# Kernel tuning notes

Measured on AMD Instinct MI355X. Metric: run time of the kernel, lower is better.

The kernel has to match this reference:

```python
import jax, jax.numpy as jnp
import numpy as np

NEG_SLOPE = 0.2  # PyG GATConv default negative_slope


def _gat_layer(x, src, dst, W, a_src, a_dst, b, num_nodes):
    # x: [N, Fin] -> h: [N, Fout]
    h = x @ W
    # per-node attention logits (heads=1)
    alpha_s = h @ a_src  # [N]
    alpha_d = h @ a_dst  # [N]
    # edge scores e_ij = LeakyReLU(a_src . h_j + a_dst . h_i), j=src, i=dst
    e = alpha_s[src] + alpha_d[dst]
    e = jnp.where(e >= 0, e, NEG_SLOPE * e)
    # segment softmax over edges sharing the same destination node
    e_max = jax.ops.segment_max(e, dst, num_segments=num_nodes)  # [N]
    w = jnp.exp(e - e_max[dst])  # [E]
    denom = jax.ops.segment_sum(w, dst, num_segments=num_nodes)  # [N]
    alpha = w / denom[dst]  # [E]
    # weighted scatter-sum of source messages into destinations
    out = jax.ops.segment_sum(h[src] * alpha[:, None], dst, num_segments=num_nodes)
    return out + b


def _add_self_loops(edge_index, num_nodes):
    loops = jnp.arange(num_nodes, dtype=edge_index.dtype)
    src = jnp.concatenate([edge_index[0], loops])
    dst = jnp.concatenate([edge_index[1], loops])
    return src, dst


def setup_inputs() -> dict:
    key = jax.random.key(0)
    ks = jax.random.split(key, 8)
    N, E, F_in, F_hid, F_out = 50000, 800000, 128, 128, 64
    inp = {
        "node_features": jax.random.normal(ks[0], (N, F_in), dtype=jnp.float32),
        "edge_index": jax.random.randint(ks[1], (2, E), 0, N, dtype=jnp.int32),
        "W1": jax.random.normal(ks[2], (F_in, F_hid), dtype=jnp.float32) / np.sqrt(F_in),
        "a_src1": jax.random.normal(ks[3], (F_hid,), dtype=jnp.float32) / np.sqrt(F_hid),
        "a_dst1": jax.random.normal(ks[4], (F_hid,), dtype=jnp.float32) / np.sqrt(F_hid),
        "b1": jnp.zeros((F_hid,), dtype=jnp.float32),
        "W2": jax.random.normal(ks[5], (F_hid, F_out), dtype=jnp.float32) / np.sqrt(F_hid),
        "a_src2": jax.random.normal(ks[6], (F_out,), dtype=jnp.float32) / np.sqrt(F_out),
        "a_dst2": jax.random.normal(ks[7], (F_out,), dtype=jnp.float32) / np.sqrt(F_out),
        "b2": jnp.zeros((F_out,), dtype=jnp.float32),
    }
    return inp


def reference(node_features, edge_index, W1, a_src1, a_dst1, b1, W2, a_src2, a_dst2, b2):
    num_nodes = node_features.shape[0]
    src, dst = _add_self_loops(edge_index, num_nodes)
    x = _gat_layer(node_features, src, dst, W1, a_src1, a_dst1, b1, num_nodes)
    x = jax.nn.relu(x)
    x = _gat_layer(x, src, dst, W2, a_src2, a_dst2, b2, num_nodes)
    return x
```

## Files before the change

### kernel.cpp

```cpp
#include <hip/hip_runtime.h>
#include <hip/hip_fp16.h>
#include <cstddef>

#define NEG_SLOPE 0.2f
#define TILE 4096
#define CSR_CAP 6144

typedef _Float16 h8 __attribute__((ext_vector_type(8)));
typedef _Float16 h4 __attribute__((ext_vector_type(4)));
typedef float f4 __attribute__((ext_vector_type(4)));

__device__ __forceinline__ float leaky(float x) { return x >= 0.f ? x : NEG_SLOPE * x; }

__device__ __forceinline__ int wave_iscan(int v, int lane) {
#pragma unroll
    for (int off = 1; off < 64; off <<= 1) {
        int t = __shfl_up(v, off);
        if (lane >= off) v += t;
    }
    return v;
}

__global__ __launch_bounds__(256) void prep(
    const float* __restrict__ W1, const float* __restrict__ W2,
    _Float16* __restrict__ W1t, _Float16* __restrict__ W2t,
    int* __restrict__ bfill)
{
    const int b = blockIdx.x;
    const int tid = threadIdx.x;
    if (b == 0) bfill[tid] = 0;
    if (b < 8) {
        for (int i = b * 2048 + tid; i < (b + 1) * 2048; i += 256) {
            int n = i >> 7, k = i & 127;
            W1t[n * 128 + k] = (_Float16)W1[k * 128 + n];
        }
    } else {
        const int bb = b - 8;
        for (int i = bb * 2048 + tid; i < (bb + 1) * 2048; i += 256) {
            int n = i >> 7, k = i & 127;
            W2t[n * 128 + k] = (_Float16)W2[k * 64 + n];
        }
    }
}

__global__ __launch_bounds__(256) void gemm1_scatter(
    const float* __restrict__ x, const _Float16* __restrict__ Wg,
    const float* __restrict__ a_s, const float* __restrict__ a_d,
    _Float16* __restrict__ hh, float* __restrict__ alphaS, float* __restrict__ alphaD,
    int N, int nblk_gemm,
    const int* __restrict__ src, const int* __restrict__ dst,
    int* __restrict__ bfill, unsigned* __restrict__ staging, int cap, int E)
{
    constexpr int K = 128;
    constexpr int LDK = K + 8;
    constexpr int F = 128;
    constexpr int NT = F / 16;

    __shared__ union {
        struct { _Float16 As[64 * LDK]; _Float16 Wt[F * LDK]; } g;
        struct {
            int lcnt[256]; int loff[256]; int gbase[256]; int ws[4];
            unsigned pairs[TILE]; unsigned char bkt[TILE];
        } s;
    } u;

    const int tid = threadIdx.x;

    if (blockIdx.x < (unsigned)nblk_gemm) {
        const int wave = tid >> 6;
        const int lane = tid & 63;
        const int q = lane >> 4;
        const int c = lane & 15;
        const int rowb = blockIdx.x * 64;

        for (int i = tid; i < 64 * (K / 4); i += 256) {
            int r = i >> 5, c4 = i & 31;
            int gr = rowb + r;
            float4 v = (gr < N) ? *(const float4*)(x + (size_t)gr * K + c4 * 4)
                                : make_float4(0.f, 0.f, 0.f, 0.f);
            h4 hv = { (_Float16)v.x, (_Float16)v.y, (_Float16)v.z, (_Float16)v.w };
            *(h4*)(u.g.As + r * LDK + c4 * 4) = hv;
        }
        for (int i = tid; i < F * (K / 8); i += 256) {
            int n = i >> 4, k8 = i & 15;
            *(h8*)(u.g.Wt + n * LDK + k8 * 8) = *(const h8*)(Wg + n * 128 + k8 * 8);
        }
        __syncthreads();

        f4 acc[NT];
#pragma unroll
        for (int nt = 0; nt < NT; nt++) acc[nt] = (f4)0.f;

        const _Float16* aw = u.g.As + (wave * 16 + c) * LDK + q * 8;
#pragma unroll
        for (int kt = 0; kt < 4; kt++) {
            h8 af = *(const h8*)(aw + kt * 32);
#pragma unroll
            for (int nt = 0; nt < NT; nt++) {
                h8 bf = *(const h8*)(u.g.Wt + (nt * 16 + c) * LDK + kt * 32 + q * 8);
                acc[nt] = __builtin_amdgcn_mfma_f32_16x16x32_f16(af, bf, acc[nt], 0, 0, 0);
            }
        }

        float asl[NT], adl[NT];
#pragma unroll
        for (int nt = 0; nt < NT; nt++) {
            asl[nt] = a_s[nt * 16 + c];
            adl[nt] = a_d[nt * 16 + c];
        }
        const int row0 = rowb + wave * 16 + q * 4;
#pragma unroll
        for (int r = 0; r < 4; r++) {
            int row = row0 + r;
            if (row < N) {
                float ps = 0.f, pd = 0.f;
#pragma unroll
                for (int nt = 0; nt < NT; nt++) {
                    float v = acc[nt][r];
                    hh[(size_t)row * F + nt * 16 + c] = (_Float16)v;
                    ps += v * asl[nt];
                    pd += v * adl[nt];
                }
#pragma unroll
                for (int off = 8; off >= 1; off >>= 1) {
                    ps += __shfl_down(ps, off, 16);
                    pd += __shfl_down(pd, off, 16);
                }
                if (c == 0) { alphaS[row] = ps; alphaD[row] = pd; }
            }
        }
    } else {
        const int base = (blockIdx.x - nblk_gemm) * TILE;
        const int vt = min(TILE, E - base);

        u.s.lcnt[tid] = 0;
        __syncthreads();

        int d[TILE / 256], s[TILE / 256], r[TILE / 256];
#pragma unroll
        for (int j = 0; j < TILE / 256; j++) {
            int idx = base + j * 256 + tid;
            if (idx < E) {
                d[j] = dst[idx]; s[j] = src[idx];
                r[j] = atomicAdd(&u.s.lcnt[d[j] >> 8], 1);
            } else d[j] = -1;
        }
        __syncthreads();
        {
            int lane = tid & 63, wid = tid >> 6;
            int v = u.s.lcnt[tid];
            int incl = wave_iscan(v, lane);
            if (lane == 63) u.s.ws[wid] = incl;
            __syncthreads();
            int woff = 0;
            for (int w = 0; w < wid; w++) woff += u.s.ws[w];
            u.s.loff[tid] = woff + incl - v;
        }
        __syncthreads();
        {
            int c = u.s.lcnt[tid];
            if (c > 0) u.s.gbase[tid] = tid * cap + atomicAdd(&bfill[tid], c);
        }
        __syncthreads();
#pragma unroll
        for (int j = 0; j < TILE / 256; j++) {
            if (d[j] >= 0) {
                int b = d[j] >> 8;
                int slot = u.s.loff[b] + r[j];
                u.s.pairs[slot] = ((unsigned)d[j] << 16) | (unsigned)s[j];
                u.s.bkt[slot] = (unsigned char)b;
            }
        }
        __syncthreads();
        for (int slot = tid; slot < vt; slot += 256) {
            int b = u.s.bkt[slot];
            staging[u.s.gbase[b] + (slot - u.s.loff[b])] = u.s.pairs[slot];
        }
    }
}

__global__ __launch_bounds__(512) void bucket_to_csr(
    const unsigned* __restrict__ staging, const int* __restrict__ bfill,
    int* __restrict__ row_start, int* __restrict__ row_end,
    int* __restrict__ src_sorted, int cap, int N)
{
    __shared__ unsigned lp[CSR_CAP];
    __shared__ int lcnt[256], loff[256], lfill[256];
    __shared__ int ws[4];
    const int tid = threadIdx.x;
    const int b = blockIdx.x;
    const int beg = b * cap;
    const int len = bfill[b];

    if (tid < 256) lcnt[tid] = 0;
    __syncthreads();
    for (int p = tid; p < len; p += 512) {
        unsigned u = staging[beg + p];
        lp[p] = u;
        atomicAdd(&lcnt[(u >> 16) & 255], 1);
    }
    __syncthreads();
    {
        int lane = tid & 63, wid = tid >> 6;
        int v = 0, incl = 0;
        if (tid < 256) {
            v = lcnt[tid];
            incl = wave_iscan(v, lane);
            if (lane == 63) ws[wid] = incl;
        }
        __syncthreads();
        if (tid < 256) {
            int woff = 0;
            for (int w = 0; w < wid; w++) woff += ws[w];
            int excl = woff + incl - v;
            loff[tid] = excl;
            lfill[tid] = excl;
            int node = (b << 8) + tid;
            if (node < N) { row_start[node] = beg + excl; row_end[node] = beg + excl + v; }
        }
    }
    __syncthreads();
    for (int p = tid; p < len; p += 512) {
        unsigned u = lp[p];
        int pos = atomicAdd(&lfill[(u >> 16) & 255], 1);
        src_sorted[beg + pos] = (int)(u & 0xFFFFu);
    }
}

template <int F, typename IT>
__global__ __launch_bounds__(256) void gemm_mfma(
    const IT* __restrict__ x, const _Float16* __restrict__ Wg,
    const float* __restrict__ a_s, const float* __restrict__ a_d,
    _Float16* __restrict__ hh, float* __restrict__ alphaS, float* __restrict__ alphaD,
    int N)
{
    constexpr int K = 128;
    constexpr int LDK = K + 8;
    constexpr int NT = F / 16;

    __shared__ _Float16 As[64 * LDK];
    __shared__ _Float16 Wt[F * LDK];

    const int tid = threadIdx.x;
    const int wave = tid >> 6;
    const int lane = tid & 63;
    const int q = lane >> 4;
    const int c = lane & 15;
    const int rowb = blockIdx.x * 64;

    if constexpr (sizeof(IT) == 4) {
        for (int i = tid; i < 64 * (K / 4); i += 256) {
            int r = i >> 5, c4 = i & 31;
            int gr = rowb + r;
            float4 v = (gr < N) ? *(const float4*)((const float*)x + (size_t)gr * K + c4 * 4)
                                : make_float4(0.f, 0.f, 0.f, 0.f);
            h4 hv = { (_Float16)v.x, (_Float16)v.y, (_Float16)v.z, (_Float16)v.w };
            *(h4*)(As + r * LDK + c4 * 4) = hv;
        }
    } else {
        for (int i = tid; i < 64 * (K / 8); i += 256) {
            int r = i >> 4, c8 = i & 15;
            int gr = rowb + r;
            h8 v;
            if (gr < N) v = *(const h8*)((const _Float16*)x + (size_t)gr * K + c8 * 8);
            else        v = (h8)(_Float16)0.f;
            *(h8*)(As + r * LDK + c8 * 8) = v;
        }
    }
    for (int i = tid; i < F * (K / 8); i += 256) {
        int n = i >> 4, k8 = i & 15;
        *(h8*)(Wt + n * LDK + k8 * 8) = *(const h8*)(Wg + n * 128 + k8 * 8);
    }
    __syncthreads();

    f4 acc[NT];
#pragma unroll
    for (int nt = 0; nt < NT; nt++) acc[nt] = (f4)0.f;

    const _Float16* aw = As + (wave * 16 + c) * LDK + q * 8;
#pragma unroll
    for (int kt = 0; kt < 4; kt++) {
        h8 af = *(const h8*)(aw + kt * 32);
#pragma unroll
        for (int nt = 0; nt < NT; nt++) {
            h8 bf = *(const h8*)(Wt + (nt * 16 + c) * LDK + kt * 32 + q * 8);
            acc[nt] = __builtin_amdgcn_mfma_f32_16x16x32_f16(af, bf, acc[nt], 0, 0, 0);
        }
    }

    float asl[NT], adl[NT];
#pragma unroll
    for (int nt = 0; nt < NT; nt++) {
        asl[nt] = a_s[nt * 16 + c];
        adl[nt] = a_d[nt * 16 + c];
    }
    const int row0 = rowb + wave * 16 + q * 4;
#pragma unroll
    for (int r = 0; r < 4; r++) {
        int row = row0 + r;
        if (row < N) {
            float ps = 0.f, pd = 0.f;
#pragma unroll
            for (int nt = 0; nt < NT; nt++) {
                float v = acc[nt][r];
                hh[(size_t)row * F + nt * 16 + c] = (_Float16)v;
                ps += v * asl[nt];
                pd += v * adl[nt];
            }
#pragma unroll
            for (int off = 8; off >= 1; off >>= 1) {
                ps += __shfl_down(ps, off, 16);
                pd += __shfl_down(pd, off, 16);
            }
            if (c == 0) { alphaS[row] = ps; alphaD[row] = pd; }
        }
    }
}

#define EDGE_BODY(SV, ACC, DEN)                                              \
    if (SV >= 0) {                                                           \
        float w = __expf(leaky(aS[SV] + adi));                               \
        uint4 uu = *(const uint4*)(hh + (size_t)SV * F + l * 8);             \
        const __half2* hp = (const __half2*)&uu;                             \
        _Pragma("unroll")                                                    \
        for (int q = 0; q < 4; q++) {                                        \
            float2 f = __half22float2(hp[q]);                                \
            ACC[q * 2] += w * f.x; ACC[q * 2 + 1] += w * f.y;                 \
        }                                                                    \
        DEN += w;                                                            \
    }

template <int F, int NS, bool RELU, typename OT>
__global__ __launch_bounds__(256) void gat_aggregate(
    const int* __restrict__ row_start, const int* __restrict__ row_end,
    const int* __restrict__ src_sorted, const __half* __restrict__ hh,
    const float* __restrict__ aS, const float* __restrict__ aD,
    const float* __restrict__ bias, OT* __restrict__ out, int N)
{
    constexpr int LPE = F / 8;
    constexpr int EPW = 64 / LPE;
    constexpr int WIN = NS * EPW;

    const int i = blockIdx.x * 4 + (threadIdx.x >> 6);
    if (i >= N) return;
    const int lane = threadIdx.x & 63;
    const int sub = lane / LPE;
    const int l = lane % LPE;

    const float adi = aD[i];
    const int start = row_start[i];
    const int end = row_end[i];

    float accA[8], accB[8];
#pragma unroll
    for (int q = 0; q < 8; q++) { accA[q] = 0.f; accB[q] = 0.f; }
    float denA = 0.f, denB = 0.f;

    int e = start + sub;
    int s0 = (e + 0 * EPW < end) ? src_sorted[e + 0 * EPW] : -1;
    int s1 = (e + 1 * EPW < end) ? src_sorted[e + 1 * EPW] : -1;
    int s2 = (e + 2 * EPW < end) ? src_sorted[e + 2 * EPW] : -1;
    int s3 = (e + 3 * EPW < end) ? src_sorted[e + 3 * EPW] : -1;
    int s4 = -1, s5 = -1, s6 = -1, s7 = -1;
    if constexpr (NS == 8) {
        s4 = (e + 4 * EPW < end) ? src_sorted[e + 4 * EPW] : -1;
        s5 = (e + 5 * EPW < end) ? src_sorted[e + 5 * EPW] : -1;
        s6 = (e + 6 * EPW < end) ? src_sorted[e + 6 * EPW] : -1;
        s7 = (e + 7 * EPW < end) ? src_sorted[e + 7 * EPW] : -1;
    }

    while (s0 >= 0) {
        int eb = e + WIN;
        int n0 = (eb + 0 * EPW < end) ? src_sorted[eb + 0 * EPW] : -1;
        int n1 = (eb + 1 * EPW < end) ? src_sorted[eb + 1 * EPW] : -1;
        int n2 = (eb + 2 * EPW < end) ? src_sorted[eb + 2 * EPW] : -1;
        int n3 = (eb + 3 * EPW < end) ? src_sorted[eb + 3 * EPW] : -1;
        int n4 = -1, n5 = -1, n6 = -1, n7 = -1;
        if constexpr (NS == 8) {
            n4 = (eb + 4 * EPW < end) ? src_sorted[eb + 4 * EPW] : -1;
            n5 = (eb + 5 * EPW < end) ? src_sorted[eb + 5 * EPW] : -1;
            n6 = (eb + 6 * EPW < end) ? src_sorted[eb + 6 * EPW] : -1;
            n7 = (eb + 7 * EPW < end) ? src_sorted[eb + 7 * EPW] : -1;
        }

        EDGE_BODY(s0, accA, denA)
        EDGE_BODY(s1, accB, denB)
        EDGE_BODY(s2, accA, denA)
        EDGE_BODY(s3, accB, denB)
        if constexpr (NS == 8) {
            EDGE_BODY(s4, accA, denA)
            EDGE_BODY(s5, accB, denB)
            EDGE_BODY(s6, accA, denA)
            EDGE_BODY(s7, accB, denB)
        }

        e = eb;
        s0 = n0; s1 = n1; s2 = n2; s3 = n3;
        if constexpr (NS == 8) { s4 = n4; s5 = n5; s6 = n6; s7 = n7; }
    }

    float acc[8];
#pragma unroll
    for (int q = 0; q < 8; q++) acc[q] = accA[q] + accB[q];
    float denom = denA + denB;

#pragma unroll
    for (int off = 32; off >= LPE; off >>= 1) {
#pragma unroll
        for (int q = 0; q < 8; q++) acc[q] += __shfl_down(acc[q], off);
        denom += __shfl_down(denom, off);
    }

    if (sub == 0) {
        float wsf = __expf(leaky(aS[i] + adi));
        uint4 u = *(const uint4*)(hh + (size_t)i * F + l * 8);
        const __half2* hp = (const __half2*)&u;
        float inv = 1.f / (denom + wsf);
        float4 b0 = *(const float4*)(bias + l * 8);
        float4 b1 = *(const float4*)(bias + l * 8 + 4);
        float o[8];
#pragma unroll
        for (int q = 0; q < 4; q++) {
            float2 f = __half22float2(hp[q]);
            o[q * 2]     = (acc[q * 2]     + wsf * f.x) * inv;
            o[q * 2 + 1] = (acc[q * 2 + 1] + wsf * f.y) * inv;
        }
        o[0] += b0.x; o[1] += b0.y; o[2] += b0.z; o[3] += b0.w;
        o[4] += b1.x; o[5] += b1.y; o[6] += b1.z; o[7] += b1.w;
        if (RELU) {
#pragma unroll
            for (int q = 0; q < 8; q++) o[q] = fmaxf(o[q], 0.f);
        }
        if constexpr (sizeof(OT) == 2) {
            __half2 qh[4];
            qh[0] = __floats2half2_rn(o[0], o[1]);
            qh[1] = __floats2half2_rn(o[2], o[3]);
            qh[2] = __floats2half2_rn(o[4], o[5]);
            qh[3] = __floats2half2_rn(o[6], o[7]);
            *(uint4*)((__half*)out + (size_t)i * F + l * 8) = *(uint4*)qh;
        } else {
            *(float4*)((float*)out + (size_t)i * F + l * 8)     = make_float4(o[0], o[1], o[2], o[3]);
            *(float4*)((float*)out + (size_t)i * F + l * 8 + 4) = make_float4(o[4], o[5], o[6], o[7]);
        }
    }
}

extern "C" void kernel_launch(void* const* d_in, const int* in_sizes, int n_in,
                              void* d_out, int out_size, void* d_ws, size_t ws_size,
                              hipStream_t stream)
{
    const float* x   = (const float*)d_in[0];
    const int*   ei  = (const int*)d_in[1];
    const float* W1  = (const float*)d_in[2];
    const float* aS1 = (const float*)d_in[3];
    const float* aD1 = (const float*)d_in[4];
    const float* b1  = (const float*)d_in[5];
    const float* W2  = (const float*)d_in[6];
    const float* aS2 = (const float*)d_in[7];
    const float* aD2 = (const float*)d_in[8];
    const float* b2  = (const float*)d_in[9];

    const int K = 128, F1 = 128, F2 = 64;
    const int N = in_sizes[0] / K;
    const int E = in_sizes[1] / 2;
    const int* src = ei;
    const int* dst = ei + E;

    const int Np = (N + 4) & ~3;
    const int NB = (N + 255) >> 8;
    const int nbt = (E + TILE - 1) / TILE;
    const int nblk_gemm = (N + 63) / 64;
    int cap = (((E / NB) * 3) / 2 + 255) & ~255;
    if (cap > CSR_CAP) cap = CSR_CAP;

    char* wsb = (char*)d_ws;
    int* bfill        = (int*)wsb;      wsb += 256 * 4;
    _Float16* W1t     = (_Float16*)wsb; wsb += 128 * 128 * 2;
    _Float16* W2t     = (_Float16*)wsb; wsb += 64 * 128 * 2;
    int* row_start    = (int*)wsb;      wsb += (size_t)Np * 4;
    int* row_end      = (int*)wsb;      wsb += (size_t)Np * 4;
    unsigned* staging = (unsigned*)wsb; wsb += (size_t)NB * CSR_CAP * 4;
    int* src_sorted   = (int*)wsb;      wsb += (size_t)NB * CSR_CAP * 4;
    _Float16* hh1     = (_Float16*)wsb; wsb += (size_t)N * F1 * 2;
    _Float16* x2h     = (_Float16*)wsb; wsb += (size_t)N * F1 * 2;
    _Float16* hh2     = (_Float16*)wsb; wsb += (size_t)N * F2 * 2;
    float* as_        = (float*)wsb;    wsb += (size_t)Np * 4;
    float* ad_        = (float*)wsb;    wsb += (size_t)Np * 4;
    float* as2_       = (float*)wsb;    wsb += (size_t)Np * 4;
    float* ad2_       = (float*)wsb;    wsb += (size_t)Np * 4;

    dim3 blk(256);

    prep<<<dim3(12), blk, 0, stream>>>(W1, W2, W1t, W2t, bfill);

    gemm1_scatter<<<dim3(nblk_gemm + nbt), blk, 0, stream>>>(
        x, W1t, aS1, aD1, hh1, as_, ad_, N, nblk_gemm,
        src, dst, bfill, staging, cap, E);

    bucket_to_csr<<<dim3(NB), dim3(512), 0, stream>>>(staging, bfill, row_start, row_end,
                                                      src_sorted, cap, N);

    gat_aggregate<F1, 8, true, __half><<<dim3((N + 3) / 4), blk, 0, stream>>>(
        row_start, row_end, src_sorted, (const __half*)hh1, as_, ad_, b1,
        (__half*)x2h, N);

    gemm_mfma<F2, _Float16><<<dim3((N + 63) / 64), blk, 0, stream>>>(
        x2h, W2t, aS2, aD2, hh2, as2_, ad2_, N);

    gat_aggregate<F2, 4, false, float><<<dim3((N + 3) / 4), blk, 0, stream>>>(
        row_start, row_end, src_sorted, (const __half*)hh2, as2_, ad2_, b2,
        (float*)d_out, N);
}
```

Before: 194.9 us.

## Precompute layer-1 edge weights and denominators during CSR build

The CSR construction kernel now computes each edge's unnormalized attention weight for layer 1, stores it next to the source index as an int2, and accumulates per-destination denominators in shared memory. The layer-1 aggregation then reads these precomputed weights instead of gathering alpha_s and calling exp per edge. The cost is a doubled edge-array footprint (8 bytes per edge), which layer 2 also pays because it reads only the .x field of the same int2 array. The max-subtraction was already absent, so numerics are unchanged apart from the order of the denominator sums.

```diff
diff --git a/kernel.cpp b/kernel.cpp
--- a/kernel.cpp
+++ b/kernel.cpp
@@ -182,17 +182,20 @@
 __global__ __launch_bounds__(512) void bucket_to_csr(
     const unsigned* __restrict__ staging, const int* __restrict__ bfill,
     int* __restrict__ row_start, int* __restrict__ row_end,
-    int* __restrict__ src_sorted, int cap, int N)
+    int2* __restrict__ sw_sorted, float* __restrict__ denom1,
+    const float* __restrict__ aS1, const float* __restrict__ aD1,
+    int cap, int N)
 {
     __shared__ unsigned lp[CSR_CAP];
     __shared__ int lcnt[256], loff[256], lfill[256];
+    __shared__ float dsum[256];
     __shared__ int ws[4];
     const int tid = threadIdx.x;
     const int b = blockIdx.x;
     const int beg = b * cap;
     const int len = bfill[b];
 
-    if (tid < 256) lcnt[tid] = 0;
+    if (tid < 256) { lcnt[tid] = 0; dsum[tid] = 0.f; }
     __syncthreads();
     for (int p = tid; p < len; p += 512) {
         unsigned u = staging[beg + p];
@@ -222,8 +225,17 @@
     __syncthreads();
     for (int p = tid; p < len; p += 512) {
         unsigned u = lp[p];
-        int pos = atomicAdd(&lfill[(u >> 16) & 255], 1);
-        src_sorted[beg + pos] = (int)(u & 0xFFFFu);
+        int node = (u >> 16) & 255;
+        int s = (int)(u & 0xFFFFu);
+        int pos = atomicAdd(&lfill[node], 1);
+        float w = __expf(leaky(aS1[s] + aD1[(b << 8) + node]));
+        sw_sorted[beg + pos] = make_int2(s, __float_as_int(w));
+        atomicAdd(&dsum[node], w);
+    }
+    __syncthreads();
+    if (tid < 256) {
+        int node = (b << 8) + tid;
+        if (node < N) denom1[node] = dsum[tid];
     }
 }
 
@@ -317,10 +329,99 @@
     }
 }
 
+__global__ __launch_bounds__(256) void gat_aggregate_pre(
+    const int* __restrict__ row_start, const int* __restrict__ row_end,
+    const int2* __restrict__ sw, const __half* __restrict__ hh,
+    const float* __restrict__ denom1,
+    const float* __restrict__ aS, const float* __restrict__ aD,
+    const float* __restrict__ bias, __half* __restrict__ out, int N)
+{
+    const int i = blockIdx.x * 4 + (threadIdx.x >> 6);
+    if (i >= N) return;
+    const int lane = threadIdx.x & 63;
+    const int sub = lane >> 4;
+    const int l = lane & 15;
+
+    const int start = row_start[i];
+    const int end = row_end[i];
+
+    float accA[8], accB[8];
+#pragma unroll
+    for (int q = 0; q < 8; q++) { accA[q] = 0.f; accB[q] = 0.f; }
+
+    const int2 none = make_int2(-1, 0);
+    int e = start + sub;
+    int2 p0 = (e + 0 * 4 < end) ? sw[e + 0 * 4] : none;
+    int2 p1 = (e + 1 * 4 < end) ? sw[e + 1 * 4] : none;
+    int2 p2 = (e + 2 * 4 < end) ? sw[e + 2 * 4] : none;
+    int2 p3 = (e + 3 * 4 < end) ? sw[e + 3 * 4] : none;
+
+    while (p0.x >= 0) {
+        int eb = e + 16;
+        int2 n0 = (eb + 0 * 4 < end) ? sw[eb + 0 * 4] : none;
+        int2 n1 = (eb + 1 * 4 < end) ? sw[eb + 1 * 4] : none;
+        int2 n2 = (eb + 2 * 4 < end) ? sw[eb + 2 * 4] : none;
+        int2 n3 = (eb + 3 * 4 < end) ? sw[eb + 3 * 4] : none;
+
+#define PRE_BODY(P, ACC)                                                     \
+        if (P.x >= 0) {                                                      \
+            float w = __int_as_float(P.y);                                   \
+            uint4 uu = *(const uint4*)(hh + (size_t)P.x * 128 + l * 8);      \
+            const __half2* hp = (const __half2*)&uu;                         \
+            _Pragma("unroll")                                                \
+            for (int q = 0; q < 4; q++) {                                    \
+                float2 f = __half22float2(hp[q]);                            \
+                ACC[q * 2] += w * f.x; ACC[q * 2 + 1] += w * f.y;             \
+            }                                                                \
+        }
+
+        PRE_BODY(p0, accA)
+        PRE_BODY(p1, accB)
+        PRE_BODY(p2, accA)
+        PRE_BODY(p3, accB)
+#undef PRE_BODY
+
+        e = eb;
+        p0 = n0; p1 = n1; p2 = n2; p3 = n3;
+    }
+
+    float acc[8];
+#pragma unroll
+    for (int q = 0; q < 8; q++) acc[q] = accA[q] + accB[q];
+
+#pragma unroll
+    for (int off = 32; off >= 16; off >>= 1) {
+#pragma unroll
+        for (int q = 0; q < 8; q++) acc[q] += __shfl_down(acc[q], off);
+    }
+
+    if (sub == 0) {
+        float wsf = __expf(leaky(aS[i] + aD[i]));
+        uint4 u = *(const uint4*)(hh + (size_t)i * 128 + l * 8);
+        const __half2* hp = (const __half2*)&u;
+        float inv = 1.f / (denom1[i] + wsf);
+        float4 b0 = *(const float4*)(bias + l * 8);
+        float4 b1v = *(const float4*)(bias + l * 8 + 4);
+        float o[8];
+#pragma unroll
+        for (int q = 0; q < 4; q++) {
+            float2 f = __half22float2(hp[q]);
+            o[q * 2]     = (acc[q * 2]     + wsf * f.x) * inv;
+            o[q * 2 + 1] = (acc[q * 2 + 1] + wsf * f.y) * inv;
+        }
+        o[0] += b0.x; o[1] += b0.y; o[2] += b0.z; o[3] += b0.w;
+        o[4] += b1v.x; o[5] += b1v.y; o[6] += b1v.z; o[7] += b1v.w;
+        h8 hv;
+#pragma unroll
+        for (int q = 0; q < 8; q++) hv[q] = (_Float16)fmaxf(o[q], 0.f);
+        *(h8*)(out + (size_t)i * 128 + l * 8) = hv;
+    }
+}
+
 #define EDGE_BODY(SV, ACC, DEN)                                              \
     if (SV >= 0) {                                                           \
         float w = __expf(leaky(aS[SV] + adi));                               \
-        uint4 uu = *(const uint4*)(hh + (size_t)SV * F + l * 8);             \
+        uint4 uu = *(const uint4*)(hh + (size_t)SV * 64 + l * 8);            \
         const __half2* hp = (const __half2*)&uu;                             \
         _Pragma("unroll")                                                    \
         for (int q = 0; q < 4; q++) {                                        \
@@ -330,22 +431,19 @@
         DEN += w;                                                            \
     }
 
-template <int F, int NS, bool RELU, typename OT>
-__global__ __launch_bounds__(256) void gat_aggregate(
+__global__ __launch_bounds__(256) void gat_aggregate2(
     const int* __restrict__ row_start, const int* __restrict__ row_end,
-    const int* __restrict__ src_sorted, const __half* __restrict__ hh,
+    const int2* __restrict__ sw, const __half* __restrict__ hh,
     const float* __restrict__ aS, const float* __restrict__ aD,
-    const float* __restrict__ bias, OT* __restrict__ out, int N)
-{
-    constexpr int LPE = F / 8;
-    constexpr int EPW = 64 / LPE;
-    constexpr int WIN = NS * EPW;
+    const float* __restrict__ bias, float* __restrict__ out, int N)
+{
+    constexpr int EPW = 8;
 
     const int i = blockIdx.x * 4 + (threadIdx.x >> 6);
     if (i >= N) return;
     const int lane = threadIdx.x & 63;
-    const int sub = lane / LPE;
-    const int l = lane % LPE;
+    const int sub = lane >> 3;
+    const int l = lane & 7;
 
     const float adi = aD[i];
     const int start = row_start[i];
@@ -357,46 +455,25 @@
     float denA = 0.f, denB = 0.f;
 
     int e = start + sub;
-    int s0 = (e + 0 * EPW < end) ? src_sorted[e + 0 * EPW] : -1;
-    int s1 = (e + 1 * EPW < end) ? src_sorted[e + 1 * EPW] : -1;
-    int s2 = (e + 2 * EPW < end) ? src_sorted[e + 2 * EPW] : -1;
-    int s3 = (e + 3 * EPW < end) ? src_sorted[e + 3 * EPW] : -1;
-    int s4 = -1, s5 = -1, s6 = -1, s7 = -1;
-    if constexpr (NS == 8) {
-        s4 = (e + 4 * EPW < end) ? src_sorted[e + 4 * EPW] : -1;
-        s5 = (e + 5 * EPW < end) ? src_sorted[e + 5 * EPW] : -1;
-        s6 = (e + 6 * EPW < end) ? src_sorted[e + 6 * EPW] : -1;
-        s7 = (e + 7 * EPW < end) ? src_sorted[e + 7 * EPW] : -1;
-    }
+    int s0 = (e + 0 * EPW < end) ? sw[e + 0 * EPW].x : -1;
+    int s1 = (e + 1 * EPW < end) ? sw[e + 1 * EPW].x : -1;
+    int s2 = (e + 2 * EPW < end) ? sw[e + 2 * EPW].x : -1;
+    int s3 = (e + 3 * EPW < end) ? sw[e + 3 * EPW].x : -1;
 
     while (s0 >= 0) {
-        int eb = e + WIN;
-        int n0 = (eb + 0 * EPW < end) ? src_sorted[eb + 0 * EPW] : -1;
-        int n1 = (eb + 1 * EPW < end) ? src_sorted[eb + 1 * EPW] : -1;
-        int n2 = (eb + 2 * EPW < end) ? src_sorted[eb + 2 * EPW] : -1;
-        int n3 = (eb + 3 * EPW < end) ? src_sorted[eb + 3 * EPW] : -1;
-        int n4 = -1, n5 = -1, n6 = -1, n7 = -1;
-        if constexpr (NS == 8) {
-            n4 = (eb + 4 * EPW < end) ? src_sorted[eb + 4 * EPW] : -1;
-            n5 = (eb + 5 * EPW < end) ? src_sorted[eb + 5 * EPW] : -1;
-            n6 = (eb + 6 * EPW < end) ? src_sorted[eb + 6 * EPW] : -1;
-            n7 = (eb + 7 * EPW < end) ? src_sorted[eb + 7 * EPW] : -1;
-        }
+        int eb = e + 4 * EPW;
+        int n0 = (eb + 0 * EPW < end) ? sw[eb + 0 * EPW].x : -1;
+        int n1 = (eb + 1 * EPW < end) ? sw[eb + 1 * EPW].x : -1;
+        int n2 = (eb + 2 * EPW < end) ? sw[eb + 2 * EPW].x : -1;
+        int n3 = (eb + 3 * EPW < end) ? sw[eb + 3 * EPW].x : -1;
 
         EDGE_BODY(s0, accA, denA)
         EDGE_BODY(s1, accB, denB)
         EDGE_BODY(s2, accA, denA)
         EDGE_BODY(s3, accB, denB)
-        if constexpr (NS == 8) {
-            EDGE_BODY(s4, accA, denA)
-            EDGE_BODY(s5, accB, denB)
-            EDGE_BODY(s6, accA, denA)
-            EDGE_BODY(s7, accB, denB)
-        }
 
         e = eb;
         s0 = n0; s1 = n1; s2 = n2; s3 = n3;
-        if constexpr (NS == 8) { s4 = n4; s5 = n5; s6 = n6; s7 = n7; }
     }
 
     float acc[8];
@@ -405,7 +482,7 @@
     float denom = denA + denB;
 
 #pragma unroll
-    for (int off = 32; off >= LPE; off >>= 1) {
+    for (int off = 32; off >= 8; off >>= 1) {
 #pragma unroll
         for (int q = 0; q < 8; q++) acc[q] += __shfl_down(acc[q], off);
         denom += __shfl_down(denom, off);
@@ -413,7 +490,7 @@
 
     if (sub == 0) {
         float wsf = __expf(leaky(aS[i] + adi));
-        uint4 u = *(const uint4*)(hh + (size_t)i * F + l * 8);
+        uint4 u = *(const uint4*)(hh + (size_t)i * 64 + l * 8);
         const __half2* hp = (const __half2*)&u;
         float inv = 1.f / (denom + wsf);
         float4 b0 = *(const float4*)(bias + l * 8);
@@ -427,21 +504,8 @@
         }
         o[0] += b0.x; o[1] += b0.y; o[2] += b0.z; o[3] += b0.w;
         o[4] += b1.x; o[5] += b1.y; o[6] += b1.z; o[7] += b1.w;
-        if (RELU) {
-#pragma unroll
-            for (int q = 0; q < 8; q++) o[q] = fmaxf(o[q], 0.f);
-        }
-        if constexpr (sizeof(OT) == 2) {
-            __half2 qh[4];
-            qh[0] = __floats2half2_rn(o[0], o[1]);
-            qh[1] = __floats2half2_rn(o[2], o[3]);
-            qh[2] = __floats2half2_rn(o[4], o[5]);
-            qh[3] = __floats2half2_rn(o[6], o[7]);
-            *(uint4*)((__half*)out + (size_t)i * F + l * 8) = *(uint4*)qh;
-        } else {
-            *(float4*)((float*)out + (size_t)i * F + l * 8)     = make_float4(o[0], o[1], o[2], o[3]);
-            *(float4*)((float*)out + (size_t)i * F + l * 8 + 4) = make_float4(o[4], o[5], o[6], o[7]);
-        }
+        *(float4*)(out + (size_t)i * 64 + l * 8)     = make_float4(o[0], o[1], o[2], o[3]);
+        *(float4*)(out + (size_t)i * 64 + l * 8 + 4) = make_float4(o[4], o[5], o[6], o[7]);
     }
 }
 
@@ -480,7 +544,8 @@
     int* row_start    = (int*)wsb;      wsb += (size_t)Np * 4;
     int* row_end      = (int*)wsb;      wsb += (size_t)Np * 4;
     unsigned* staging = (unsigned*)wsb; wsb += (size_t)NB * CSR_CAP * 4;
-    int* src_sorted   = (int*)wsb;      wsb += (size_t)NB * CSR_CAP * 4;
+    int2* sw_sorted   = (int2*)wsb;     wsb += (size_t)NB * CSR_CAP * 8;
+    float* denom1     = (float*)wsb;    wsb += (size_t)Np * 4;
     _Float16* hh1     = (_Float16*)wsb; wsb += (size_t)N * F1 * 2;
     _Float16* x2h     = (_Float16*)wsb; wsb += (size_t)N * F1 * 2;
     _Float16* hh2     = (_Float16*)wsb; wsb += (size_t)N * F2 * 2;
@@ -497,17 +562,17 @@
         x, W1t, aS1, aD1, hh1, as_, ad_, N, nblk_gemm,
         src, dst, bfill, staging, cap, E);
 
-    bucket_to_csr<<<dim3(NB), dim3(512), 0, stream>>>(staging, bfill, row_start, row_end,
-                                                      src_sorted, cap, N);
-
-    gat_aggregate<F1, 8, true, __half><<<dim3((N + 3) / 4), blk, 0, stream>>>(
-        row_start, row_end, src_sorted, (const __half*)hh1, as_, ad_, b1,
+    bucket_to_csr<<<dim3(NB), dim3(512), 0, stream>>>(
+        staging, bfill, row_start, row_end, sw_sorted, denom1, as_, ad_, cap, N);
+
+    gat_aggregate_pre<<<dim3((N + 3) / 4), blk, 0, stream>>>(
+        row_start, row_end, sw_sorted, (const __half*)hh1, denom1, as_, ad_, b1,
         (__half*)x2h, N);
 
     gemm_mfma<F2, _Float16><<<dim3((N + 63) / 64), blk, 0, stream>>>(
         x2h, W2t, aS2, aD2, hh2, as2_, ad2_, N);
 
-    gat_aggregate<F2, 4, false, float><<<dim3((N + 3) / 4), blk, 0, stream>>>(
-        row_start, row_end, src_sorted, (const __half*)hh2, as2_, ad2_, b2,
+    gat_aggregate2<<<dim3((N + 3) / 4), blk, 0, stream>>>(
+        row_start, row_end, sw_sorted, (const __half*)hh2, as2_, ad2_, b2,
         (float*)d_out, N);
 }
```

After: 204.5 us. 4.9% more time.
